# Optimization experiments

Hardware: AMD Instinct MI355X
Metric: run time of the kernel (lower is better)

Reference implementation:

```python
import jax, jax.numpy as jnp
import numpy as np

INF = 10000.0  # matches the module's soft -inf


def setup_inputs() -> dict:
    key = jax.random.key(0)
    B, S, n_labels, n_tags = 128, 1024, 64, 256
    k0, k1, k2, k3, k4 = jax.random.split(key, 5)
    x = jax.random.normal(k0, (B, S, n_labels), dtype=jnp.float32)
    tag2label = jax.random.randint(k1, (n_tags,), 0, n_labels)
    y = jax.random.randint(k2, (B, S), 0, n_tags)
    label_transitions = 0.1 * jax.random.normal(k3, (n_labels, n_labels), dtype=jnp.float32)
    # automaton transition constraints: allowed (0.0) or forbidden (-INF)
    allowed = jax.random.bernoulli(k4, 0.3, (n_tags, n_tags)) | jnp.eye(n_tags, dtype=bool)
    transition_constraints = jnp.where(allowed, 0.0, -INF).astype(jnp.float32)
    start_mask = jnp.arange(n_tags) < 32            # tags reachable from the start state
    end_mask = jnp.arange(n_tags) >= n_tags - 32    # tags ending in an accepting state
    return dict(x=x, y=y, label_transitions=label_transitions,
                transition_constraints=transition_constraints,
                tag2label=tag2label, start_mask=start_mask, end_mask=end_mask)


def reference(x, y, label_transitions, transition_constraints, tag2label, start_mask, end_mask):
    # _transitions(): expand label-level transitions to tag pairs, add constraints
    transitions = label_transitions[tag2label][:, tag2label] + transition_constraints  # [T, T]
    # x[:, :, tag2label] as in log_p/loss
    xt = x[:, :, tag2label]  # [B, S, T]

    # ---- _logZ: sequential log-semiring matmul recurrence ----
    init = jnp.where(start_mask, xt[:, 0, :], -INF)  # [B, T]

    def step(logits, xi):
        # logmmexp(logits, transitions) + xi
        new = jax.nn.logsumexp(logits[:, :, None] + transitions[None, :, :], axis=1) + xi
        return new, None

    final, _ = jax.lax.scan(step, init, jnp.swapaxes(xt, 0, 1)[1:])  # scan over S-1 steps
    final = jnp.where(end_mask, final, -INF)
    logZ = jax.nn.logsumexp(final, axis=1)  # [B]

    # ---- _score: gold-path emission + transition scores ----
    emis = jnp.take_along_axis(xt, y[:, :, None], axis=2)[..., 0].sum(axis=1)  # [B]
    trans = transitions[y[:, :-1], y[:, 1:]].sum(axis=1)                        # [B]
    score = emis + trans

    # loss(): mean NLL
    return jnp.mean(logZ - score)
```

## Files before the change

kernel.cpp:

```cpp
#include <hip/hip_runtime.h>

#define Bb 128
#define Ss 1024
#define NL 64
#define NT 256
#define CH 128
#define DCH 8
#define VW 2
#define STRDB 272
#define PBUFB (16 * STRDB)
#define XSTR 68
#define LOGF128 4.852030263919617f

typedef float f32x4 __attribute__((ext_vector_type(4)));
typedef unsigned long long u64;

#define BARRIER() asm volatile("s_waitcnt lgkmcnt(0)\ns_barrier" ::: "memory")

__device__ __forceinline__ int slotfn(int p) {
  return (p & 0xC0) | (((p & 3) << 4) | ((p & 63) >> 2));
}
__device__ __forceinline__ float dec8(unsigned char b) {
  int e = (b >> 3) & 15, m = b & 7;
  float v = e ? ldexpf((float)(8 + m), e - 10) : ldexpf((float)m, -9);
  return (b & 0x80) ? -v : v;
}
__device__ __forceinline__ unsigned int pk8lo(float a, float b) {
  return (unsigned int)__builtin_amdgcn_cvt_pk_fp8_f32(a, b, 0, false) & 0xffffu;
}

template <int ctrl, int rmask>
__device__ __forceinline__ float dpp_add(float x) {
  int y = __builtin_amdgcn_update_dpp(0, __builtin_bit_cast(int, x), ctrl, rmask, 0xf, true);
  return x + __builtin_bit_cast(float, y);
}
template <int ctrl, int rmask>
__device__ __forceinline__ float dpp_max(float x) {
  int y = __builtin_amdgcn_update_dpp(0, __builtin_bit_cast(int, x), ctrl, rmask, 0xf, true);
  return fmaxf(x, __builtin_bit_cast(float, y));
}
__device__ __forceinline__ float wsum16(float v) {
  v = dpp_add<0x111, 0xf>(v);
  v = dpp_add<0x112, 0xf>(v);
  v = dpp_add<0x114, 0xf>(v);
  v = dpp_add<0x118, 0xf>(v);
  return v;
}
__device__ __forceinline__ float wmax16(float v) {
  v = dpp_max<0x111, 0xf>(v);
  v = dpp_max<0x112, 0xf>(v);
  v = dpp_max<0x114, 0xf>(v);
  v = dpp_max<0x118, 0xf>(v);
  return v;
}
__device__ __forceinline__ float wave_sum_shfl(float v) {
#pragma unroll
  for (int off = 32; off > 0; off >>= 1) v += __shfl_xor(v, off, 64);
  return v;
}

__global__ void prep0_k(const int* __restrict__ t2l, int* __restrict__ Tg,
                        int* __restrict__ Lab) {
  __shared__ int cnt[NL], off[NL];
  int t = threadIdx.x;
  if (t < NL) cnt[t] = 0;
  __syncthreads();
  int lab = t2l[t];
  atomicAdd(&cnt[lab], 1);
  __syncthreads();
  if (t == 0) {
    int a = 0;
    for (int l = 0; l < NL; ++l) { off[l] = a; a += cnt[l]; }
  }
  __syncthreads();
  if (t < NL) cnt[t] = off[t];
  __syncthreads();
  int slot = atomicAdd(&cnt[lab], 1);
  Tg[slot] = t;
  Lab[slot] = lab;
}

__global__ void prepw_k(const float* __restrict__ L, const float* __restrict__ C,
                        const int* __restrict__ t2l, const int* __restrict__ Tg,
                        const int* __restrict__ Lab, unsigned char* __restrict__ Wf) {
  int p = blockIdx.x, n = threadIdx.x;
  int ktag = Tg[slotfn(p)];
  float t = L[t2l[ktag] * NL + Lab[n]] + C[ktag * NT + Tg[n]];
  float w = __expf(t);
  Wf[n * NT + p] = (unsigned char)(pk8lo(w, w) & 0xff);
}

__global__ void prept_k(const float* __restrict__ L, const float* __restrict__ C,
                        const int* __restrict__ t2l, float* __restrict__ T) {
  int i = blockIdx.x, j = threadIdx.x;
  T[i * NT + j] = L[t2l[i] * NL + t2l[j]] + C[i * NT + j];
}

__global__ __launch_bounds__(256, 2) void scan_k(
    const float* __restrict__ x, const int* __restrict__ y,
    const int* __restrict__ t2l, const unsigned char* __restrict__ Wf,
    const float* __restrict__ T, const int* __restrict__ Tgg,
    const int* __restrict__ Labg, float* __restrict__ Ls, float* __restrict__ Sc) {
  const int blk = blockIdx.x;
  const bool c0 = blk < 8;
  const int c = c0 ? 0 : (blk - 8) / 8 + 1;
  const int b0 = c0 ? blk * 16 : ((blk - 8) % 8) * 16;
  const int sbase = c0 ? 0 : c * DCH - VW;
  const int i0 = c0 ? 1 : 0;
  const int ilast = c0 ? DCH - 1 : VW + DCH - 1;
  const int accfrom = c0 ? 1 : VW + 1;

  const int t = threadIdx.x;
  const int w = t >> 6;
  const int l15 = t & 15;
  const int q = (t >> 4) & 3;

  __shared__ __align__(16) unsigned char PbF[2 * PBUFB];
  __shared__ __align__(16) float Sp[2][16][4];
  __shared__ __align__(16) float Xe[2][16][XSTR];
  __shared__ float Xm[2][16];
  __shared__ int TgS[NT], LabS[NT];
  __shared__ float rowsum[16];

  TgS[t] = Tgg[t];
  LabS[t] = Labg[t];
  __syncthreads();

  {
    int sl = t & 15, ms = t >> 4;
    int bsc = b0 + ms;
    float sc = 0.f;
    if (sl < DCH) {
      int s = c * DCH + sl;
      const int* yb = y + bsc * Ss;
      int ys = yb[s];
      sc = x[(size_t)bsc * (Ss * NL) + s * NL + t2l[ys]];
      if (s >= 1) sc += T[yb[s - 1] * NT + ys];
    }
    sc = wsum16(sc);
    if (sl == 15) Sc[c * Bb + bsc] = sc;
  }

  u64 bfv[4][8];
  int labv[4];
#pragma unroll
  for (int t4 = 0; t4 < 4; ++t4) {
    int n = w * 64 + t4 * 16 + l15;
    labv[t4] = LabS[n];
    const u64* wp = (const u64*)(Wf + n * NT + q * 64);
#pragma unroll
    for (int f = 0; f < 8; ++f) bfv[t4][f] = wp[f];
  }

  {
    int mi = t >> 4;
    int pstart = (t & 15) * 16;
    float ps = 0.f;
#pragma unroll
    for (int g = 0; g < 4; ++g) {
      unsigned int wd = 0;
#pragma unroll
      for (int bb = 0; bb < 4; ++bb) {
        int p = pstart + g * 4 + bb;
        float v;
        if (c0) {
          int sl = slotfn(p);
          v = (TgS[sl] < 32)
                  ? __expf(x[(size_t)(b0 + mi) * (Ss * NL) + LabS[sl]])
                  : 0.f;
        } else {
          v = 1.0f;
        }
        ps += v;
        wd |= (pk8lo(v, v) & 0xffu) << (8 * bb);
      }
      *(unsigned int*)&PbF[mi * STRDB + pstart + g * 4] = wd;
    }
    ps = wsum16(ps);
    if ((t & 15) == 15) {
      Sp[0][mi][0] = ps; Sp[0][mi][1] = 0.f; Sp[0][mi][2] = 0.f; Sp[0][mi][3] = 0.f;
    }
  }

  const int mi = t >> 4;
  const int c4 = (t & 15) * 4;
  const float* xbase = x + (size_t)(b0 + mi) * (Ss * NL) + c4;
  auto ldx = [&](int i) -> float4 {
    int ii = i < ilast ? i : ilast;
    return *(const float4*)(xbase + (size_t)(sbase + ii) * NL);
  };
  {
    float4 xf = ldx(i0);
    float4 ef;
    ef.x = __expf(xf.x); ef.y = __expf(xf.y);
    ef.z = __expf(xf.z); ef.w = __expf(xf.w);
    *(float4*)&Xe[0][mi][c4] = ef;
    float mxl = fmaxf(fmaxf(ef.x, ef.y), fmaxf(ef.z, ef.w));
    mxl = wmax16(mxl);
    if ((t & 15) == 15) Xm[0][mi] = mxl;
  }
  float4 xrA = ldx(i0 + 1);
  float4 xrB = ldx(i0 + 2);
  int lexp[4] = {0, 0, 0, 0};
  float lsm[4] = {1.f, 1.f, 1.f, 1.f};
  __syncthreads();

#define STEP(I, PH)                                                                  \
  do {                                                                               \
    const unsigned char* ab_ = &PbF[(PH) * PBUFB + l15 * STRDB + q * 64];            \
    uint4 a0_ = *(const uint4*)(ab_ + 0);                                            \
    uint4 a1_ = *(const uint4*)(ab_ + 16);                                           \
    uint4 a2_ = *(const uint4*)(ab_ + 32);                                           \
    uint4 a3_ = *(const uint4*)(ab_ + 48);                                           \
    if ((I) < ilast) {                                                               \
      float4 ef_;                                                                    \
      ef_.x = __expf(xrA.x); ef_.y = __expf(xrA.y);                                  \
      ef_.z = __expf(xrA.z); ef_.w = __expf(xrA.w);                                  \
      *(float4*)&Xe[(PH) ^ 1][mi][c4] = ef_;                                         \
      float mxl_ = fmaxf(fmaxf(ef_.x, ef_.y), fmaxf(ef_.z, ef_.w));                  \
      mxl_ = wmax16(mxl_);                                                           \
      if ((t & 15) == 15) Xm[(PH) ^ 1][mi] = mxl_;                                   \
    }                                                                                \
    xrA = xrB;                                                                       \
    xrB = ldx((I) + 3);                                                              \
    float iS_[4];                                                                    \
    _Pragma("unroll") for (int r = 0; r < 4; ++r) {                                  \
      float4 sp = *(const float4*)&Sp[PH][4 * q + r][0];                             \
      float mxv = Xm[PH][4 * q + r];                                                 \
      float s_ = (sp.x + sp.y) + (sp.z + sp.w);                                      \
      iS_[r] = __frcp_rn(s_) * 128.0f * __frcp_rn(mxv);                              \
      if ((I) >= accfrom) {                                                          \
        int bi_ = __builtin_bit_cast(int, s_);                                       \
        lexp[r] += ((bi_ >> 23) & 255) - 127;                                        \
        lsm[r] *= __builtin_bit_cast(float, (bi_ & 0x007fffff) | 0x3f800000);        \
      }                                                                              \
      if ((I) >= accfrom - 1) {                                                      \
        int bm_ = __builtin_bit_cast(int, mxv);                                      \
        lexp[r] += ((bm_ >> 23) & 255) - 127;                                        \
        lsm[r] *= __builtin_bit_cast(float, (bm_ & 0x007fffff) | 0x3f800000);        \
      }                                                                              \
    }                                                                                \
    float E_[16];                                                                    \
    _Pragma("unroll") for (int t4 = 0; t4 < 4; ++t4)                                 \
        _Pragma("unroll") for (int r = 0; r < 4; ++r)                                \
            E_[t4 * 4 + r] = Xe[PH][4 * q + r][labv[t4]] * iS_[r];                   \
    u64 af_[8];                                                                      \
    af_[0] = a0_.x | ((u64)a0_.y << 32); af_[1] = a0_.z | ((u64)a0_.w << 32);        \
    af_[2] = a1_.x | ((u64)a1_.y << 32); af_[3] = a1_.z | ((u64)a1_.w << 32);        \
    af_[4] = a2_.x | ((u64)a2_.y << 32); af_[5] = a2_.z | ((u64)a2_.w << 32);        \
    af_[6] = a3_.x | ((u64)a3_.y << 32); af_[7] = a3_.z | ((u64)a3_.w << 32);        \
    f32x4 ac0 = {0.f, 0.f, 0.f, 0.f}, ac1 = ac0, ac2 = ac0, ac3 = ac0;               \
    _Pragma("unroll") for (int f = 0; f < 8; ++f) {                                  \
      long aa = (long)af_[f];                                                        \
      ac0 = __builtin_amdgcn_mfma_f32_16x16x32_fp8_fp8(aa, (long)bfv[0][f], ac0, 0, 0, 0); \
      ac1 = __builtin_amdgcn_mfma_f32_16x16x32_fp8_fp8(aa, (long)bfv[1][f], ac1, 0, 0, 0); \
      ac2 = __builtin_amdgcn_mfma_f32_16x16x32_fp8_fp8(aa, (long)bfv[2][f], ac2, 0, 0, 0); \
      ac3 = __builtin_amdgcn_mfma_f32_16x16x32_fp8_fp8(aa, (long)bfv[3][f], ac3, 0, 0, 0); \
    }                                                                                \
    _Pragma("unroll") for (int r = 0; r < 4; ++r) {                                  \
      float d0 = ac0[r] * E_[0 + r];                                                 \
      float d1 = ac1[r] * E_[4 + r];                                                 \
      float d2 = ac2[r] * E_[8 + r];                                                 \
      float d3 = ac3[r] * E_[12 + r];                                                \
      unsigned int wd = pk8lo(d0, d1) | (pk8lo(d2, d3) << 16);                       \
      *(unsigned int*)&PbF[((PH) ^ 1) * PBUFB + (4 * q + r) * STRDB + w * 64 +       \
                           l15 * 4] = wd;                                            \
      float pr = (d0 + d1) + (d2 + d3);                                              \
      pr = wsum16(pr);                                                               \
      if (l15 == 15) Sp[(PH) ^ 1][4 * q + r][w] = pr;                                \
    }                                                                                \
    BARRIER();                                                                       \
  } while (0)

  const int niter = ilast - i0 + 1;
  {
    int k = 0;
    for (; k + 1 < niter; k += 2) {
      STEP(i0 + k, 0);
      STEP(i0 + k + 1, 1);
    }
    if (k < niter) STEP(i0 + k, 0);
  }
#undef STEP
  const int FB = niter & 1;

  {
    int m = t >> 4;
    int pstart = (t & 15) * 16;
    const unsigned char* rp = &PbF[FB * PBUFB + m * STRDB + pstart];
    float ps = 0.f;
#pragma unroll
    for (int k = 0; k < 16; ++k) {
      int p = pstart + k;
      bool on = (c != CH - 1) || (TgS[slotfn(p)] >= 224);
      if (on) ps += dec8(rp[k]);
    }
    ps = wsum16(ps);
    if ((t & 15) == 15) rowsum[m] = ps;
  }
  __syncthreads();
  if (w == 0 && l15 == 0) {
    const float LN2 = 0.69314718056f;
    const float corr = (c0 ? (float)(DCH - 1) : (float)DCH) * LOGF128;
#pragma unroll
    for (int r = 0; r < 4; ++r)
      Ls[c * Bb + b0 + 4 * q + r] =
          (float)lexp[r] * LN2 + __logf(lsm[r]) + __logf(rowsum[4 * q + r]) - corr;
  }
}

__global__ void final_k(const float* __restrict__ Ls, const float* __restrict__ Sc,
                        float* __restrict__ out) {
  int b = threadIdx.x;
  float acc = 0.f;
#pragma unroll 8
  for (int c = 0; c < CH; ++c) acc += Ls[c * Bb + b] - Sc[c * Bb + b];
  __shared__ float p2[2];
  float ws = wave_sum_shfl(acc);
  if ((b & 63) == 0) p2[b >> 6] = ws;
  __syncthreads();
  if (b == 0) out[0] = (p2[0] + p2[1]) * (1.0f / Bb);
}

extern "C" void kernel_launch(void* const* d_in, const int* in_sizes, int n_in,
                              void* d_out, int out_size, void* d_ws, size_t ws_size,
                              hipStream_t stream) {
  const float* x = (const float*)d_in[0];
  const int* y = (const int*)d_in[1];
  const float* L = (const float*)d_in[2];
  const float* C = (const float*)d_in[3];
  const int* t2l = (const int*)d_in[4];

  char* ws = (char*)d_ws;
  float* T = (float*)ws;                  ws += NT * NT * 4;
  unsigned char* Wf = (unsigned char*)ws; ws += NT * NT;
  int* Tg = (int*)ws;                     ws += NT * 4;
  int* Lab = (int*)ws;                    ws += NT * 4;
  float* Ls = (float*)ws;                 ws += CH * Bb * 4;
  float* Sc = (float*)ws;                 ws += CH * Bb * 4;

  prep0_k<<<1, NT, 0, stream>>>(t2l, Tg, Lab);
  prepw_k<<<NT, NT, 0, stream>>>(L, C, t2l, Tg, Lab, Wf);
  prept_k<<<NT, NT, 0, stream>>>(L, C, t2l, T);
  scan_k<<<8 * CH, 256, 0, stream>>>(x, y, t2l, Wf, T, Tg, Lab, Ls, Sc);
  final_k<<<1, 128, 0, stream>>>(Ls, Sc, (float*)d_out);
}
```

Baseline: 134.3 us.

## Use 16x16x128 scaled FP8 MFMA, halve chunk count, batch log-scale folding

Replaces the eight 16x16x32 FP8 MFMAs per output tile with two 16x16x128 scaled f8f6f4 MFMAs, so operand fragments are repacked as 8-int vectors and the LDS A-fragment loads are reorganised into low and high halves. The chunk count drops from 128 to 64, each chunk now covering 16 positions, which changes how the sequence is split across workgroups. The per-step exponent/mantissa bookkeeping is simplified to a single multiply, with normalisation folded every two steps. This cuts MFMA issue count and per-step scalar work, at the cost of an overflow risk in the accumulated product and a different chunk/parallelism balance.

Result: faster. 121.8 us (-9.3%).

```diff
diff --git a/kernel.cpp b/kernel.cpp
--- a/kernel.cpp
+++ b/kernel.cpp
@@ -4,8 +4,8 @@
 #define Ss 1024
 #define NL 64
 #define NT 256
-#define CH 128
-#define DCH 8
+#define CH 64
+#define DCH 16
 #define VW 2
 #define STRDB 272
 #define PBUFB (16 * STRDB)
@@ -13,6 +13,7 @@
 #define LOGF128 4.852030263919617f
 
 typedef float f32x4 __attribute__((ext_vector_type(4)));
+typedef int i8v __attribute__((ext_vector_type(8)));
 typedef unsigned long long u64;
 
 #define BARRIER() asm volatile("s_waitcnt lgkmcnt(0)\ns_barrier" ::: "memory")
@@ -129,27 +130,28 @@
   {
     int sl = t & 15, ms = t >> 4;
     int bsc = b0 + ms;
-    float sc = 0.f;
-    if (sl < DCH) {
-      int s = c * DCH + sl;
-      const int* yb = y + bsc * Ss;
-      int ys = yb[s];
-      sc = x[(size_t)bsc * (Ss * NL) + s * NL + t2l[ys]];
-      if (s >= 1) sc += T[yb[s - 1] * NT + ys];
-    }
+    int s = c * DCH + sl;
+    const int* yb = y + bsc * Ss;
+    int ys = yb[s];
+    float sc = x[(size_t)bsc * (Ss * NL) + s * NL + t2l[ys]];
+    if (s >= 1) sc += T[yb[s - 1] * NT + ys];
     sc = wsum16(sc);
     if (sl == 15) Sc[c * Bb + bsc] = sc;
   }
 
-  u64 bfv[4][8];
+  i8v bfv[4][2];
   int labv[4];
 #pragma unroll
   for (int t4 = 0; t4 < 4; ++t4) {
     int n = w * 64 + t4 * 16 + l15;
     labv[t4] = LabS[n];
-    const u64* wp = (const u64*)(Wf + n * NT + q * 64);
-#pragma unroll
-    for (int f = 0; f < 8; ++f) bfv[t4][f] = wp[f];
+#pragma unroll
+    for (int h = 0; h < 2; ++h) {
+      const uint4* wp = (const uint4*)(Wf + n * NT + h * 128 + q * 32);
+      uint4 u0 = wp[0], u1 = wp[1];
+      bfv[t4][h] = (i8v){(int)u0.x, (int)u0.y, (int)u0.z, (int)u0.w,
+                         (int)u1.x, (int)u1.y, (int)u1.z, (int)u1.w};
+    }
   }
 
   {
@@ -207,11 +209,11 @@
 
 #define STEP(I, PH)                                                                  \
   do {                                                                               \
-    const unsigned char* ab_ = &PbF[(PH) * PBUFB + l15 * STRDB + q * 64];            \
-    uint4 a0_ = *(const uint4*)(ab_ + 0);                                            \
-    uint4 a1_ = *(const uint4*)(ab_ + 16);                                           \
-    uint4 a2_ = *(const uint4*)(ab_ + 32);                                           \
-    uint4 a3_ = *(const uint4*)(ab_ + 48);                                           \
+    const unsigned char* ab_ = &PbF[(PH) * PBUFB + l15 * STRDB + q * 32];            \
+    uint4 al0 = *(const uint4*)(ab_);                                                \
+    uint4 al1 = *(const uint4*)(ab_ + 16);                                           \
+    uint4 ah0 = *(const uint4*)(ab_ + 128);                                          \
+    uint4 ah1 = *(const uint4*)(ab_ + 144);                                          \
     if ((I) < ilast) {                                                               \
       float4 ef_;                                                                    \
       ef_.x = __expf(xrA.x); ef_.y = __expf(xrA.y);                                  \
@@ -228,35 +230,36 @@
       float4 sp = *(const float4*)&Sp[PH][4 * q + r][0];                             \
       float mxv = Xm[PH][4 * q + r];                                                 \
       float s_ = (sp.x + sp.y) + (sp.z + sp.w);                                      \
-      iS_[r] = __frcp_rn(s_) * 128.0f * __frcp_rn(mxv);                              \
-      if ((I) >= accfrom) {                                                          \
-        int bi_ = __builtin_bit_cast(int, s_);                                       \
-        lexp[r] += ((bi_ >> 23) & 255) - 127;                                        \
-        lsm[r] *= __builtin_bit_cast(float, (bi_ & 0x007fffff) | 0x3f800000);        \
-      }                                                                              \
-      if ((I) >= accfrom - 1) {                                                      \
-        int bm_ = __builtin_bit_cast(int, mxv);                                      \
-        lexp[r] += ((bm_ >> 23) & 255) - 127;                                        \
-        lsm[r] *= __builtin_bit_cast(float, (bm_ & 0x007fffff) | 0x3f800000);        \
-      }                                                                              \
+      float sm_ = s_ * mxv;                                                          \
+      iS_[r] = 128.0f * __frcp_rn(sm_);                                              \
+      if ((I) >= accfrom) lsm[r] *= sm_;                                             \
+      else if ((I) == accfrom - 1) lsm[r] *= mxv;                                    \
     }                                                                                \
     float E_[16];                                                                    \
     _Pragma("unroll") for (int t4 = 0; t4 < 4; ++t4)                                 \
         _Pragma("unroll") for (int r = 0; r < 4; ++r)                                \
             E_[t4 * 4 + r] = Xe[PH][4 * q + r][labv[t4]] * iS_[r];                   \
-    u64 af_[8];                                                                      \
-    af_[0] = a0_.x | ((u64)a0_.y << 32); af_[1] = a0_.z | ((u64)a0_.w << 32);        \
-    af_[2] = a1_.x | ((u64)a1_.y << 32); af_[3] = a1_.z | ((u64)a1_.w << 32);        \
-    af_[4] = a2_.x | ((u64)a2_.y << 32); af_[5] = a2_.z | ((u64)a2_.w << 32);        \
-    af_[6] = a3_.x | ((u64)a3_.y << 32); af_[7] = a3_.z | ((u64)a3_.w << 32);        \
+    i8v alo = (i8v){(int)al0.x, (int)al0.y, (int)al0.z, (int)al0.w,                  \
+                    (int)al1.x, (int)al1.y, (int)al1.z, (int)al1.w};                 \
+    i8v ahi = (i8v){(int)ah0.x, (int)ah0.y, (int)ah0.z, (int)ah0.w,                  \
+                    (int)ah1.x, (int)ah1.y, (int)ah1.z, (int)ah1.w};                 \
     f32x4 ac0 = {0.f, 0.f, 0.f, 0.f}, ac1 = ac0, ac2 = ac0, ac3 = ac0;               \
-    _Pragma("unroll") for (int f = 0; f < 8; ++f) {                                  \
-      long aa = (long)af_[f];                                                        \
-      ac0 = __builtin_amdgcn_mfma_f32_16x16x32_fp8_fp8(aa, (long)bfv[0][f], ac0, 0, 0, 0); \
-      ac1 = __builtin_amdgcn_mfma_f32_16x16x32_fp8_fp8(aa, (long)bfv[1][f], ac1, 0, 0, 0); \
-      ac2 = __builtin_amdgcn_mfma_f32_16x16x32_fp8_fp8(aa, (long)bfv[2][f], ac2, 0, 0, 0); \
-      ac3 = __builtin_amdgcn_mfma_f32_16x16x32_fp8_fp8(aa, (long)bfv[3][f], ac3, 0, 0, 0); \
-    }                                                                                \
+    ac0 = __builtin_amdgcn_mfma_scale_f32_16x16x128_f8f6f4(                          \
+        alo, bfv[0][0], ac0, 0, 0, 0, 0x7f, 0, 0x7f);                                \
+    ac1 = __builtin_amdgcn_mfma_scale_f32_16x16x128_f8f6f4(                          \
+        alo, bfv[1][0], ac1, 0, 0, 0, 0x7f, 0, 0x7f);                                \
+    ac2 = __builtin_amdgcn_mfma_scale_f32_16x16x128_f8f6f4(                          \
+        alo, bfv[2][0], ac2, 0, 0, 0, 0x7f, 0, 0x7f);                                \
+    ac3 = __builtin_amdgcn_mfma_scale_f32_16x16x128_f8f6f4(                          \
+        alo, bfv[3][0], ac3, 0, 0, 0, 0x7f, 0, 0x7f);                                \
+    ac0 = __builtin_amdgcn_mfma_scale_f32_16x16x128_f8f6f4(                          \
+        ahi, bfv[0][1], ac0, 0, 0, 0, 0x7f, 0, 0x7f);                                \
+    ac1 = __builtin_amdgcn_mfma_scale_f32_16x16x128_f8f6f4(                          \
+        ahi, bfv[1][1], ac1, 0, 0, 0, 0x7f, 0, 0x7f);                                \
+    ac2 = __builtin_amdgcn_mfma_scale_f32_16x16x128_f8f6f4(                          \
+        ahi, bfv[2][1], ac2, 0, 0, 0, 0x7f, 0, 0x7f);                                \
+    ac3 = __builtin_amdgcn_mfma_scale_f32_16x16x128_f8f6f4(                          \
+        ahi, bfv[3][1], ac3, 0, 0, 0, 0x7f, 0, 0x7f);                                \
     _Pragma("unroll") for (int r = 0; r < 4; ++r) {                                  \
       float d0 = ac0[r] * E_[0 + r];                                                 \
       float d1 = ac1[r] * E_[4 + r];                                                 \
@@ -272,14 +275,27 @@
     BARRIER();                                                                       \
   } while (0)
 
+#define FOLDLOG()                                                                    \
+  do {                                                                               \
+    _Pragma("unroll") for (int r = 0; r < 4; ++r) {                                  \
+      int bi_ = __builtin_bit_cast(int, lsm[r]);                                     \
+      lexp[r] += ((bi_ >> 23) & 255) - 127;                                          \
+      lsm[r] = __builtin_bit_cast(float, (bi_ & 0x007fffff) | 0x3f800000);           \
+    }                                                                                \
+  } while (0)
+
   const int niter = ilast - i0 + 1;
   {
     int k = 0;
     for (; k + 1 < niter; k += 2) {
       STEP(i0 + k, 0);
       STEP(i0 + k + 1, 1);
-    }
-    if (k < niter) STEP(i0 + k, 0);
+      FOLDLOG();
+    }
+    if (k < niter) {
+      STEP(i0 + k, 0);
+      FOLDLOG();
+    }
   }
 #undef STEP
   const int FB = niter & 1;
```
